# Optimization experiments

Hardware: AMD Instinct MI355X
Metric: run time of the kernel (lower is better)

Reference implementation:

```python
import jax, jax.numpy as jnp
import numpy as np

B, N, D = 64, 197, 768
H, E, R = 12, 8, 8


def setup_inputs() -> dict:
    key = jax.random.key(0)
    ks = jax.random.split(key, 8)
    s = 0.02
    return {
        "tokens": jax.random.normal(ks[0], (B, N, D), dtype=jnp.float32),
        "qkv_w": jax.random.normal(ks[1], (3 * D, D), dtype=jnp.float32) * s,
        "qkv_b": jax.random.normal(ks[2], (3 * D,), dtype=jnp.float32) * s,
        "proj_w": jax.random.normal(ks[3], (D, D), dtype=jnp.float32) * s,
        "proj_b": jax.random.normal(ks[4], (D,), dtype=jnp.float32) * s,
        "gate_w": jax.random.normal(ks[5], (E, D), dtype=jnp.float32) * s,
        "lora_a": jax.random.normal(ks[6], (E, D, R), dtype=jnp.float32) * s,
        "lora_b": jax.random.normal(ks[7], (E, R, 3 * D), dtype=jnp.float32) * s,
    }


def reference(tokens, qkv_w, qkv_b, proj_w, proj_b, gate_w, lora_a, lora_b):
    b, n, d = tokens.shape
    hd = d // H
    scale = hd ** (-0.5)
    # frozen qkv projection: [b, n, 3d]
    qkv = jnp.einsum("bnd,kd->bnk", tokens, qkv_w) + qkv_b
    # LoRA-MoE delta (soft router over experts)
    gates = jax.nn.softmax(jnp.einsum("bnd,ed->bne", tokens, gate_w), axis=-1)
    h = jnp.einsum("bnd,edr->bner", tokens, lora_a)  # [b,n,E,R]
    delta = jnp.einsum("bner,erk,bne->bnk", h, lora_b, gates)  # [b,n,3d]
    # adding delta before the reshape is identical to per-q/k/v addition after
    qkv = (qkv + delta).reshape(b, n, 3, H, hd).transpose(2, 0, 3, 1, 4)
    q, k, v = qkv[0], qkv[1], qkv[2]  # each [b,H,n,hd]
    attn = jax.nn.softmax(jnp.einsum("bhqd,bhkd->bhqk", q, k) * scale, axis=-1)
    out = jnp.einsum("bhqk,bhkd->bhqd", attn, v)
    out = out.transpose(0, 2, 1, 3).reshape(b, n, d)
    return jnp.einsum("bnd,kd->bnk", out, proj_w) + proj_b
```

## Files before the change

### kernel.cpp

```cpp
#include <hip/hip_runtime.h>
#include <hip/hip_bf16.h>

typedef __hip_bfloat16 BF16;
typedef __attribute__((ext_vector_type(8))) short bf16x8;
typedef __attribute__((ext_vector_type(4))) short bf16x4;
typedef __attribute__((ext_vector_type(4))) float f32x4;
typedef __attribute__((ext_vector_type(4))) int int4v;
typedef __attribute__((ext_vector_type(2))) int int2v;

#define MTOK 12608
#define D_IN 768
#define KAUG 832
#define N_QKV 2304

#define AS1 __attribute__((address_space(1)))
#define AS3 __attribute__((address_space(3)))
#define SB0() __builtin_amdgcn_sched_barrier(0)

#if __has_builtin(__builtin_amdgcn_mfma_f32_16x16x16bf16_1k)
__device__ __forceinline__ f32x4 mfma16(bf16x4 a, bf16x4 b, f32x4 c) {
  return __builtin_amdgcn_mfma_f32_16x16x16bf16_1k(a, b, c, 0, 0, 0);
}
#else
__device__ __forceinline__ f32x4 mfma16(bf16x4 a, bf16x4 b, f32x4 c) {
  f32x4 d;
  asm volatile("v_mfma_f32_16x16x16_bf16 %0, %1, %2, %3"
               : "=v"(d) : "v"(a), "v"(b), "0"(c));
  return d;
}
#endif

__global__ __launch_bounds__(256) void prep_all_k(const float* __restrict__ qkv_w,
                                                  const float* __restrict__ lora_b,
                                                  const float* __restrict__ proj_w,
                                                  const float* __restrict__ lora_a,
                                                  BF16* __restrict__ Waug,
                                                  BF16* __restrict__ Pb,
                                                  BF16* __restrict__ LAt) {
  int idx = blockIdx.x*256 + threadIdx.x;
  const int N1 = N_QKV*KAUG;
  const int N2 = N1 + D_IN*D_IN;
  const int N3 = N2 + 64*D_IN;
  if (idx < N1) {
    int k = idx / KAUG, c = idx - k*KAUG;
    float v = (c < D_IN) ? qkv_w[k*D_IN + c] : lora_b[(size_t)(c - D_IN)*N_QKV + k];
    Waug[idx] = (BF16)v;
  } else if (idx < N2) {
    int i = idx - N1;
    Pb[i] = (BF16)proj_w[i];
  } else if (idx < N3) {
    int i = idx - N2;
    int j = i / D_IN, d = i - j*D_IN;
    LAt[i] = (BF16)lora_a[(size_t)(j >> 3)*6144 + d*8 + (j & 7)];
  }
}

__global__ __launch_bounds__(256) void token_prep_k(const float* __restrict__ tokens,
                                                    const float* __restrict__ gate_w,
                                                    BF16* __restrict__ Aaug,
                                                    float* __restrict__ gates) {
  int w = blockIdx.x*4 + (threadIdx.x >> 6);
  int lane = threadIdx.x & 63;
  if (w >= MTOK) return;
  const float4* x4 = (const float4*)(tokens + (size_t)w*D_IN);
  float4 xv[3];
  #pragma unroll
  for (int i=0;i<3;++i) xv[i] = x4[lane + 64*i];
  #pragma unroll
  for (int i=0;i<3;++i) {
    ushort4 u;
    BF16 b0 = (BF16)xv[i].x, b1 = (BF16)xv[i].y, b2 = (BF16)xv[i].z, b3 = (BF16)xv[i].w;
    u.x = *(unsigned short*)&b0; u.y = *(unsigned short*)&b1;
    u.z = *(unsigned short*)&b2; u.w = *(unsigned short*)&b3;
    *(ushort4*)(Aaug + (size_t)w*KAUG + (lane + 64*i)*4) = u;
  }
  float g[8] = {0,0,0,0,0,0,0,0};
  #pragma unroll
  for (int i=0;i<3;++i) {
    const int d4 = (lane + 64*i)*4;
    #pragma unroll
    for (int e=0;e<8;++e) {
      float4 gw = *(const float4*)(gate_w + e*D_IN + d4);
      g[e] += xv[i].x*gw.x + xv[i].y*gw.y + xv[i].z*gw.z + xv[i].w*gw.w;
    }
  }
  #pragma unroll
  for (int e=0;e<8;++e) {
    #pragma unroll
    for (int off=32; off; off >>= 1) g[e] += __shfl_xor(g[e], off);
  }
  float mx = g[0];
  #pragma unroll
  for (int e=1;e<8;++e) mx = fmaxf(mx, g[e]);
  float pe[8]; float ssum = 0.f;
  #pragma unroll
  for (int e=0;e<8;++e) { pe[e] = __expf(g[e]-mx); ssum += pe[e]; }
  float inv = 1.f/ssum;
  if (lane < 8) {
    float val = 0.f;
    #pragma unroll
    for (int e=0;e<8;++e) val = (lane==e) ? pe[e]*inv : val;
    gates[(size_t)w*8 + lane] = val;
  }
}

template<int ROWS>
__device__ __forceinline__ void stage_bt(const BF16* __restrict__ g, int ldg, int row0, int M,
                                         BF16* lds, int kbase, int t) {
  constexpr int NIT = ROWS*8/256;
  #pragma unroll
  for (int it=0; it<NIT; ++it) {
    int c = it*256 + t;
    int r = c >> 3, kc = c & 7;
    int rg = row0 + r;
    rg = (rg < M) ? rg : (M-1);
    const BF16* gp = g + (size_t)rg*ldg + kbase + kc*8;
    BF16* lp = lds + (it*256 + (t & ~63))*8;
    __builtin_amdgcn_global_load_lds((const AS1 void*)gp, (AS3 void*)lp, 16, 0, 0);
  }
}

template<int BM, int BN, int EPI>
__global__ __launch_bounds__(256,3) void gemm_bt_k(const BF16* __restrict__ A, int lda,
                                                   const BF16* __restrict__ Bt, int ldb,
                                                   const float* __restrict__ aux,
                                                   void* __restrict__ Cv, int ldc,
                                                   int M, int K) {
  constexpr int BK = 64;
  constexpr int WM = BM/2, WN = BN/2;
  constexpr int MF = WM/16, NF = WN/16;
  __shared__ BF16 Al[BM*BK];
  __shared__ BF16 Bl[BN*BK];
  const int n0 = blockIdx.x*BN, m0 = blockIdx.y*BM;
  const int t = threadIdx.x, lane = t & 63, wid = t >> 6;
  const int wm = (wid >> 1)*WM, wn = (wid & 1)*WN;
  f32x4 acc[MF][NF] = {};
  const int KT = K/BK;
  for (int kt=0; kt<KT; ++kt) {
    stage_bt<BM>(A, lda, m0, M, Al, kt*BK, t);
    stage_bt<BN>(Bt, ldb, n0, 1<<30, Bl, kt*BK, t);
    __syncthreads();
    #pragma unroll
    for (int kk=0; kk<2; ++kk) {
      bf16x8 a[MF], b[NF];
      const int col = kk*32 + (lane >> 4)*8;
      #pragma unroll
      for (int m=0;m<MF;++m) a[m] = *(const bf16x8*)(Al + (wm + m*16 + (lane & 15))*BK + col);
      #pragma unroll
      for (int n=0;n<NF;++n) b[n] = *(const bf16x8*)(Bl + (wn + n*16 + (lane & 15))*BK + col);
      #pragma unroll
      for (int m=0;m<MF;++m)
        #pragma unroll
        for (int n=0;n<NF;++n)
          acc[m][n] = __builtin_amdgcn_mfma_f32_16x16x32_bf16(a[m], b[n], acc[m][n], 0, 0, 0);
    }
    __syncthreads();
  }
  #pragma unroll
  for (int m=0;m<MF;++m) {
    #pragma unroll
    for (int n=0;n<NF;++n) {
      const int rb = m0 + wm + m*16 + (lane >> 4)*4;
      const int c = n0 + wn + n*16 + (lane & 15);
      #pragma unroll
      for (int j=0;j<4;++j) {
        const int r = rb + j;
        if (r < M) {
          float v = acc[m][n][j];
          if (EPI == 0) {
            v *= aux[(size_t)r*8 + (c >> 3)];
            ((BF16*)Cv)[(size_t)r*ldc + c] = (BF16)v;
          } else if (EPI == 1) {
            v += aux[c];
            ((BF16*)Cv)[(size_t)r*ldc + c] = (BF16)v;
          } else {
            v += aux[c];
            ((float*)Cv)[(size_t)r*ldc + c] = v;
          }
        }
      }
    }
  }
}

template<int EPI, int NBN, int LDA, int LDB, int LDC>
__global__ __launch_bounds__(256,2) void gemm2_k(const BF16* __restrict__ A,
                                                 const BF16* __restrict__ Bt,
                                                 const float* __restrict__ bias,
                                                 void* __restrict__ Cv,
                                                 int M, int K) {
  __shared__ BF16 Lsh[2][2][8192];
  const int t = threadIdx.x, lane = t & 63, wid = t >> 6;
  const int nwg = gridDim.x;
  const int q8 = nwg >> 3, r8 = nwg & 7;
  const int xcd = blockIdx.x & 7, pos = blockIdx.x >> 3;
  const int wg = (xcd < r8 ? xcd*(q8+1) : r8*(q8+1) + (xcd - r8)*q8) + pos;
  const int mb = wg / NBN, nb = wg - mb*NBN;
  const int m0 = mb*128, n0 = nb*128;
  const int KT = K/64;
  const int q4 = lane & 15;
  const int wm = (wid >> 1)*64, wn = (wid & 1)*64;

  const BF16 *sA[4], *sB[4];
  #pragma unroll
  for (int it=0; it<4; ++it) {
    int c = it*256 + t;
    int r = c >> 3, p = c & 7;
    int sc = p ^ (r & 7);
    int ra = m0 + r; ra = ra < M ? ra : M-1;
    sA[it] = A  + (size_t)ra*LDA + sc*8;
    sB[it] = Bt + (size_t)(n0 + r)*LDB + sc*8;
  }
  auto stageAB = [&](int buf, int tile) {
    #pragma unroll
    for (int it=0; it<4; ++it)
      __builtin_amdgcn_global_load_lds((const AS1 void*)(sA[it] + tile*64),
        (AS3 void*)(&Lsh[buf][0][0] + (it*256 + (t & ~63))*8), 16, 0, 0);
    #pragma unroll
    for (int it=0; it<4; ++it)
      __builtin_amdgcn_global_load_lds((const AS1 void*)(sB[it] + tile*64),
        (AS3 void*)(&Lsh[buf][1][0] + (it*256 + (t & ~63))*8), 16, 0, 0);
  };

  const int sw = (q4 & 7) << 3;
  const int ck[2] = { (((lane >> 4)*8)) ^ sw, ((32 + (lane >> 4)*8)) ^ sw };

  f32x4 acc[4][4] = {};
  stageAB(0, 0);
  asm volatile("s_waitcnt vmcnt(0)" ::: "memory"); SB0();
  __builtin_amdgcn_s_barrier();

  for (int kt = 0; kt < KT; ++kt) {
    const int buf = kt & 1;
    if (kt+1 < KT) stageAB(buf^1, kt+1);
    bf16x8 a[4][2], b[4][2];
    #pragma unroll
    for (int m=0;m<4;++m)
      #pragma unroll
      for (int kk=0;kk<2;++kk)
        a[m][kk] = *(const bf16x8*)(&Lsh[buf][0][0] + (wm + m*16 + q4)*64 + ck[kk]);
    #pragma unroll
    for (int n=0;n<4;++n)
      #pragma unroll
      for (int kk=0;kk<2;++kk)
        b[n][kk] = *(const bf16x8*)(&Lsh[buf][1][0] + (wn + n*16 + q4)*64 + ck[kk]);
    asm volatile("s_waitcnt lgkmcnt(0)" ::: "memory"); SB0();
    __builtin_amdgcn_s_setprio(1);
    #pragma unroll
    for (int kk=0;kk<2;++kk)
      #pragma unroll
      for (int m=0;m<4;++m)
        #pragma unroll
        for (int n=0;n<4;++n)
          acc[m][n] = __builtin_amdgcn_mfma_f32_16x16x32_bf16(a[m][kk], b[n][kk], acc[m][n], 0,0,0);
    __builtin_amdgcn_s_setprio(0);
    SB0();
    if (kt+1 < KT) asm volatile("s_waitcnt vmcnt(0)" ::: "memory");
    SB0();
    __builtin_amdgcn_s_barrier();
  }

  float bv[4];
  #pragma unroll
  for (int n=0;n<4;++n) bv[n] = bias[n0 + wn + n*16 + q4];
  #pragma unroll
  for (int m=0;m<4;++m) {
    #pragma unroll
    for (int j=0;j<4;++j) {
      const int r = m0 + wm + m*16 + (lane >> 4)*4 + j;
      if (r < M) {
        #pragma unroll
        for (int n=0;n<4;++n) {
          float v = acc[m][n][j] + bv[n];
          const size_t idx = (size_t)r*LDC + n0 + wn + n*16 + q4;
          if (EPI == 1) ((BF16*)Cv)[idx] = (BF16)v;
          else          ((float*)Cv)[idx] = v;
        }
      }
    }
  }
}

__device__ __forceinline__ int pack2bf(float lo, float hi) {
  BF16 a = (BF16)lo, b = (BF16)hi;
  unsigned short al = *(unsigned short*)&a, bh = *(unsigned short*)&b;
  return (int)(((unsigned)bh << 16) | (unsigned)al);
}

__global__ __launch_bounds__(256,2) void attn_k(const BF16* __restrict__ QKV,
                                                BF16* __restrict__ O) {
  constexpr int KSTR = 72;
  constexpr int VSTR = 236;
  constexpr int OSTR = 72;
  __shared__ BF16 Kl[208*KSTR];
  __shared__ BF16 Vt[64*VSTR];
  __shared__ BF16 Ol[4][16*OSTR];
  const int bh = blockIdx.x;
  const int b = bh / 12, h = bh - b*12;
  const size_t rowbase = (size_t)b*197;
  const int t = threadIdx.x, lane = t & 63, wid = t >> 6;
  const BF16 z = (BF16)0.0f;
  int4v rk[7], rv[7];
  int cc[7];
  #pragma unroll
  for (int it=0; it<7; ++it) {
    int c = t + it*256; c = (c < 1663) ? c : 1663;
    cc[it] = c;
    int r = c >> 3, kc = c & 7;
    int rr = (r < 197) ? r : 196;
    rk[it] = *(const int4v*)(QKV + (rowbase + rr)*N_QKV + 768  + h*64 + kc*8);
    rv[it] = *(const int4v*)(QKV + (rowbase + rr)*N_QKV + 1536 + h*64 + kc*8);
  }
  #pragma unroll
  for (int it=0; it<7; ++it) {
    int c = cc[it];
    int r = c >> 3, kc = c & 7;
    int4v kval = rk[it];
    if (r >= 197) { kval[0]=0; kval[1]=0; kval[2]=0; kval[3]=0; }
    *(int4v*)(Kl + r*KSTR + kc*8) = kval;
    const BF16* pv = (const BF16*)&rv[it];
    if (r < 197) {
      #pragma unroll
      for (int i=0;i<8;++i) Vt[(kc*8 + i)*VSTR + r] = pv[i];
    } else {
      #pragma unroll
      for (int i=0;i<8;++i) Vt[(kc*8 + i)*VSTR + r] = z;
    }
  }
  __syncthreads();

  const int g = lane >> 4;
  const int q4 = lane & 15;

  for (int chunk = wid; chunk < 13; chunk += 4) {
    const int q0 = chunk*16;
    int qr = q0 + q4;
    qr = (qr < 197) ? qr : 196;
    bf16x8 qa[2];
    #pragma unroll
    for (int kk=0;kk<2;++kk)
      qa[kk] = *(const bf16x8*)(QKV + (rowbase + qr)*N_QKV + h*64 + kk*32 + g*8);
    f32x4 zf = {0.f,0.f,0.f,0.f};
    f32x4 s[13];
    #pragma unroll
    for (int nf=0;nf<13;++nf) s[nf] = zf;
    #pragma unroll
    for (int nf=0;nf<13;++nf) {
      #pragma unroll
      for (int kk=0;kk<2;++kk) {
        bf16x8 kb = *(const bf16x8*)(Kl + (nf*16 + q4)*KSTR + kk*32 + g*8);
        s[nf] = __builtin_amdgcn_mfma_f32_16x16x32_bf16(kb, qa[kk], s[nf], 0, 0, 0);
      }
    }
    float m = -1e30f;
    #pragma unroll
    for (int nf=0;nf<13;++nf) {
      #pragma unroll
      for (int j=0;j<4;++j) {
        const int kg = nf*16 + g*4 + j;
        float v = s[nf][j]*0.125f;
        v = (kg < 197) ? v : -1e30f;
        s[nf][j] = v;
        m = fmaxf(m, v);
      }
    }
    m = fmaxf(m, __shfl_xor(m, 16));
    m = fmaxf(m, __shfl_xor(m, 32));
    float lsum = 0.f;
    #pragma unroll
    for (int nf=0;nf<13;++nf) {
      #pragma unroll
      for (int j=0;j<4;++j) {
        float p = __expf(s[nf][j] - m);
        s[nf][j] = p;
        lsum += p;
      }
    }
    lsum += __shfl_xor(lsum, 16);
    lsum += __shfl_xor(lsum, 32);
    bf16x4 pa[13];
    #pragma unroll
    for (int nf=0;nf<13;++nf) {
      int2v pr;
      pr[0] = pack2bf(s[nf][0], s[nf][1]);
      pr[1] = pack2bf(s[nf][2], s[nf][3]);
      pa[nf] = *(bf16x4*)&pr;
    }
    f32x4 o[4] = {};
    #pragma unroll
    for (int nf=0; nf<13; ++nf) {
      #pragma unroll
      for (int df=0; df<4; ++df) {
        bf16x4 vb = *(const bf16x4*)(Vt + (df*16 + q4)*VSTR + nf*16 + g*4);
        o[df] = mfma16(pa[nf], vb, o[df]);
      }
    }
    float ldiv[4];
    #pragma unroll
    for (int j=0;j<4;++j) ldiv[j] = __shfl(lsum, g*4 + j);
    asm volatile("s_waitcnt lgkmcnt(0)" ::: "memory"); SB0();
    #pragma unroll
    for (int df=0; df<4; ++df)
      #pragma unroll
      for (int j=0;j<4;++j)
        Ol[wid][(g*4 + j)*OSTR + df*16 + q4] = (BF16)(o[df][j] / ldiv[j]);
    asm volatile("s_waitcnt lgkmcnt(0)" ::: "memory"); SB0();
    #pragma unroll
    for (int it=0; it<2; ++it) {
      const int lr = (lane >> 3) + it*8;
      const int chk = lane & 7;
      const int r = q0 + lr;
      int4v v = *(const int4v*)(&Ol[wid][lr*OSTR + chk*8]);
      if (r < 197)
        *(int4v*)(O + (rowbase + r)*768 + h*64 + chk*8) = v;
    }
  }
}

extern "C" void kernel_launch(void* const* d_in, const int* in_sizes, int n_in,
                              void* d_out, int out_size, void* d_ws, size_t ws_size,
                              hipStream_t stream) {
  const float* tokens = (const float*)d_in[0];
  const float* qkv_w  = (const float*)d_in[1];
  const float* qkv_b  = (const float*)d_in[2];
  const float* proj_w = (const float*)d_in[3];
  const float* proj_b = (const float*)d_in[4];
  const float* gate_w = (const float*)d_in[5];
  const float* lora_a = (const float*)d_in[6];
  const float* lora_b = (const float*)d_in[7];

  size_t off = 0;
  auto take = [&](size_t bytes) {
    off = (off + 255) & ~(size_t)255;
    void* p = (char*)d_ws + off;
    off += bytes;
    return p;
  };
  BF16* Waug  = (BF16*)take((size_t)N_QKV*KAUG*2);
  BF16* Pb    = (BF16*)take((size_t)D_IN*D_IN*2);
  BF16* LAt   = (BF16*)take((size_t)64*D_IN*2);
  BF16* Aaug  = (BF16*)take((size_t)MTOK*KAUG*2);
  float* gates= (float*)take((size_t)MTOK*8*4);
  BF16* QKVb  = (BF16*)take((size_t)MTOK*N_QKV*2);
  BF16* Oc    = (BF16*)take((size_t)MTOK*D_IN*2);

  const int NPREP = N_QKV*KAUG + D_IN*D_IN + 64*D_IN;
  prep_all_k<<<(NPREP + 255)/256, 256, 0, stream>>>(
      qkv_w, lora_b, proj_w, lora_a, Waug, Pb, LAt);
  token_prep_k<<<MTOK/4, 256, 0, stream>>>(tokens, gate_w, Aaug, gates);
  gemm_bt_k<64,64,0><<<dim3(1, MTOK/64), 256, 0, stream>>>(
      Aaug, KAUG, LAt, D_IN, gates, (void*)(Aaug + 768), KAUG, MTOK, D_IN);
  gemm2_k<1, 18, KAUG, KAUG, N_QKV><<<99*18, 256, 0, stream>>>(
      Aaug, Waug, qkv_b, (void*)QKVb, MTOK, KAUG);
  attn_k<<<768, 256, 0, stream>>>(QKVb, Oc);
  gemm2_k<2, 6, D_IN, D_IN, D_IN><<<99*6, 256, 0, stream>>>(
      Oc, Pb, proj_b, d_out, MTOK, D_IN);
}
```

Baseline: 161.2 us.

## Merge weight and token prep kernels; use 160-row M tiles in GEMMs

The two preprocessing kernels become one launch, with blocks split by index between weight conversion and token conversion/gating, saving a kernel launch and letting both parts run concurrently. The bf16 GEMM kernel now takes the M tile height as a template parameter, and both the QKV and output-projection GEMMs use 160-row tiles (79 M-blocks instead of 99). This changes the workgroup count against the CU count and raises per-wave accumulator registers and LDS use, which may affect occupancy at the 2-waves launch bound.

Measured after the change: 152.6 us. -5.3%, faster.

```diff
diff --git a/kernel.cpp b/kernel.cpp
--- a/kernel.cpp
+++ b/kernel.cpp
@@ -30,36 +30,41 @@
 }
 #endif
 
-__global__ __launch_bounds__(256) void prep_all_k(const float* __restrict__ qkv_w,
+#define NPREP (N_QKV*KAUG + D_IN*D_IN + 64*D_IN)
+#define PREP_BLK ((NPREP + 255)/256)
+#define TOK_BLK (MTOK/4)
+
+__global__ __launch_bounds__(256) void prep_tok_k(const float* __restrict__ qkv_w,
                                                   const float* __restrict__ lora_b,
                                                   const float* __restrict__ proj_w,
                                                   const float* __restrict__ lora_a,
+                                                  const float* __restrict__ tokens,
+                                                  const float* __restrict__ gate_w,
                                                   BF16* __restrict__ Waug,
                                                   BF16* __restrict__ Pb,
-                                                  BF16* __restrict__ LAt) {
-  int idx = blockIdx.x*256 + threadIdx.x;
-  const int N1 = N_QKV*KAUG;
-  const int N2 = N1 + D_IN*D_IN;
-  const int N3 = N2 + 64*D_IN;
-  if (idx < N1) {
-    int k = idx / KAUG, c = idx - k*KAUG;
-    float v = (c < D_IN) ? qkv_w[k*D_IN + c] : lora_b[(size_t)(c - D_IN)*N_QKV + k];
-    Waug[idx] = (BF16)v;
-  } else if (idx < N2) {
-    int i = idx - N1;
-    Pb[i] = (BF16)proj_w[i];
-  } else if (idx < N3) {
-    int i = idx - N2;
-    int j = i / D_IN, d = i - j*D_IN;
-    LAt[i] = (BF16)lora_a[(size_t)(j >> 3)*6144 + d*8 + (j & 7)];
-  }
-}
-
-__global__ __launch_bounds__(256) void token_prep_k(const float* __restrict__ tokens,
-                                                    const float* __restrict__ gate_w,
-                                                    BF16* __restrict__ Aaug,
-                                                    float* __restrict__ gates) {
-  int w = blockIdx.x*4 + (threadIdx.x >> 6);
+                                                  BF16* __restrict__ LAt,
+                                                  BF16* __restrict__ Aaug,
+                                                  float* __restrict__ gates) {
+  if (blockIdx.x < PREP_BLK) {
+    int idx = blockIdx.x*256 + threadIdx.x;
+    const int N1 = N_QKV*KAUG;
+    const int N2 = N1 + D_IN*D_IN;
+    const int N3 = N2 + 64*D_IN;
+    if (idx < N1) {
+      int k = idx / KAUG, c = idx - k*KAUG;
+      float v = (c < D_IN) ? qkv_w[k*D_IN + c] : lora_b[(size_t)(c - D_IN)*N_QKV + k];
+      Waug[idx] = (BF16)v;
+    } else if (idx < N2) {
+      int i = idx - N1;
+      Pb[i] = (BF16)proj_w[i];
+    } else if (idx < N3) {
+      int i = idx - N2;
+      int j = i / D_IN, d = i - j*D_IN;
+      LAt[i] = (BF16)lora_a[(size_t)(j >> 3)*6144 + d*8 + (j & 7)];
+    }
+    return;
+  }
+  int w = (blockIdx.x - PREP_BLK)*4 + (threadIdx.x >> 6);
   int lane = threadIdx.x & 63;
   if (w >= MTOK) return;
   const float4* x4 = (const float4*)(tokens + (size_t)w*D_IN);
@@ -183,49 +188,58 @@
   }
 }
 
-template<int EPI, int NBN, int LDA, int LDB, int LDC>
+template<int BM, int EPI, int NBN, int LDA, int LDB, int LDC>
 __global__ __launch_bounds__(256,2) void gemm2_k(const BF16* __restrict__ A,
                                                  const BF16* __restrict__ Bt,
                                                  const float* __restrict__ bias,
                                                  void* __restrict__ Cv,
                                                  int M, int K) {
-  __shared__ BF16 Lsh[2][2][8192];
+  constexpr int MF = BM/32;
+  constexpr int NITA = BM/32;
+  __shared__ BF16 LA[2][BM*64];
+  __shared__ BF16 LB[2][8192];
   const int t = threadIdx.x, lane = t & 63, wid = t >> 6;
   const int nwg = gridDim.x;
   const int q8 = nwg >> 3, r8 = nwg & 7;
   const int xcd = blockIdx.x & 7, pos = blockIdx.x >> 3;
   const int wg = (xcd < r8 ? xcd*(q8+1) : r8*(q8+1) + (xcd - r8)*q8) + pos;
   const int mb = wg / NBN, nb = wg - mb*NBN;
-  const int m0 = mb*128, n0 = nb*128;
+  const int m0 = mb*BM, n0 = nb*128;
   const int KT = K/64;
   const int q4 = lane & 15;
-  const int wm = (wid >> 1)*64, wn = (wid & 1)*64;
-
-  const BF16 *sA[4], *sB[4];
+  const int wm = (wid >> 1)*(BM/2), wn = (wid & 1)*64;
+
+  const BF16 *sA[NITA], *sB[4];
+  #pragma unroll
+  for (int it=0; it<NITA; ++it) {
+    int c = it*256 + t;
+    int r = c >> 3, p = c & 7;
+    int sc = p ^ (r & 7);
+    int ra = m0 + r; ra = ra < M ? ra : M-1;
+    sA[it] = A + (size_t)ra*LDA + sc*8;
+  }
   #pragma unroll
   for (int it=0; it<4; ++it) {
     int c = it*256 + t;
     int r = c >> 3, p = c & 7;
     int sc = p ^ (r & 7);
-    int ra = m0 + r; ra = ra < M ? ra : M-1;
-    sA[it] = A  + (size_t)ra*LDA + sc*8;
     sB[it] = Bt + (size_t)(n0 + r)*LDB + sc*8;
   }
   auto stageAB = [&](int buf, int tile) {
     #pragma unroll
-    for (int it=0; it<4; ++it)
+    for (int it=0; it<NITA; ++it)
       __builtin_amdgcn_global_load_lds((const AS1 void*)(sA[it] + tile*64),
-        (AS3 void*)(&Lsh[buf][0][0] + (it*256 + (t & ~63))*8), 16, 0, 0);
+        (AS3 void*)(&LA[buf][0] + (it*256 + (t & ~63))*8), 16, 0, 0);
     #pragma unroll
     for (int it=0; it<4; ++it)
       __builtin_amdgcn_global_load_lds((const AS1 void*)(sB[it] + tile*64),
-        (AS3 void*)(&Lsh[buf][1][0] + (it*256 + (t & ~63))*8), 16, 0, 0);
+        (AS3 void*)(&LB[buf][0] + (it*256 + (t & ~63))*8), 16, 0, 0);
   };
 
   const int sw = (q4 & 7) << 3;
   const int ck[2] = { (((lane >> 4)*8)) ^ sw, ((32 + (lane >> 4)*8)) ^ sw };
 
-  f32x4 acc[4][4] = {};
+  f32x4 acc[MF][4] = {};
   stageAB(0, 0);
   asm volatile("s_waitcnt vmcnt(0)" ::: "memory"); SB0();
   __builtin_amdgcn_s_barrier();
@@ -233,23 +247,23 @@
   for (int kt = 0; kt < KT; ++kt) {
     const int buf = kt & 1;
     if (kt+1 < KT) stageAB(buf^1, kt+1);
-    bf16x8 a[4][2], b[4][2];
-    #pragma unroll
-    for (int m=0;m<4;++m)
+    bf16x8 a[MF][2], b[4][2];
+    #pragma unroll
+    for (int m=0;m<MF;++m)
       #pragma unroll
       for (int kk=0;kk<2;++kk)
-        a[m][kk] = *(const bf16x8*)(&Lsh[buf][0][0] + (wm + m*16 + q4)*64 + ck[kk]);
+        a[m][kk] = *(const bf16x8*)(&LA[buf][0] + (wm + m*16 + q4)*64 + ck[kk]);
     #pragma unroll
     for (int n=0;n<4;++n)
       #pragma unroll
       for (int kk=0;kk<2;++kk)
-        b[n][kk] = *(const bf16x8*)(&Lsh[buf][1][0] + (wn + n*16 + q4)*64 + ck[kk]);
+        b[n][kk] = *(const bf16x8*)(&LB[buf][0] + (wn + n*16 + q4)*64 + ck[kk]);
     asm volatile("s_waitcnt lgkmcnt(0)" ::: "memory"); SB0();
     __builtin_amdgcn_s_setprio(1);
     #pragma unroll
     for (int kk=0;kk<2;++kk)
       #pragma unroll
-      for (int m=0;m<4;++m)
+      for (int m=0;m<MF;++m)
         #pragma unroll
         for (int n=0;n<4;++n)
           acc[m][n] = __builtin_amdgcn_mfma_f32_16x16x32_bf16(a[m][kk], b[n][kk], acc[m][n], 0,0,0);
@@ -264,7 +278,7 @@
   #pragma unroll
   for (int n=0;n<4;++n) bv[n] = bias[n0 + wn + n*16 + q4];
   #pragma unroll
-  for (int m=0;m<4;++m) {
+  for (int m=0;m<MF;++m) {
     #pragma unroll
     for (int j=0;j<4;++j) {
       const int r = m0 + wm + m*16 + (lane >> 4)*4 + j;
@@ -444,15 +458,14 @@
   BF16* QKVb  = (BF16*)take((size_t)MTOK*N_QKV*2);
   BF16* Oc    = (BF16*)take((size_t)MTOK*D_IN*2);
 
-  const int NPREP = N_QKV*KAUG + D_IN*D_IN + 64*D_IN;
-  prep_all_k<<<(NPREP + 255)/256, 256, 0, stream>>>(
-      qkv_w, lora_b, proj_w, lora_a, Waug, Pb, LAt);
-  token_prep_k<<<MTOK/4, 256, 0, stream>>>(tokens, gate_w, Aaug, gates);
+  prep_tok_k<<<PREP_BLK + TOK_BLK, 256, 0, stream>>>(
+      qkv_w, lora_b, proj_w, lora_a, tokens, gate_w,
+      Waug, Pb, LAt, Aaug, gates);
   gemm_bt_k<64,64,0><<<dim3(1, MTOK/64), 256, 0, stream>>>(
       Aaug, KAUG, LAt, D_IN, gates, (void*)(Aaug + 768), KAUG, MTOK, D_IN);
-  gemm2_k<1, 18, KAUG, KAUG, N_QKV><<<99*18, 256, 0, stream>>>(
+  gemm2_k<160, 1, 18, KAUG, KAUG, N_QKV><<<79*18, 256, 0, stream>>>(
       Aaug, Waug, qkv_b, (void*)QKVb, MTOK, KAUG);
   attn_k<<<768, 256, 0, stream>>>(QKVb, Oc);
-  gemm2_k<2, 6, D_IN, D_IN, D_IN><<<99*6, 256, 0, stream>>>(
+  gemm2_k<160, 2, 6, D_IN, D_IN, D_IN><<<79*6, 256, 0, stream>>>(
       Oc, Pb, proj_b, d_out, MTOK, D_IN);
 }
```
